# Performance work log

Measured on AMD Instinct MI355X. Metric: run time of the kernel, lower is better.

Reference implementation:

```python
import jax, jax.numpy as jnp
import numpy as np

B, C, H, W = 4, 512, 64, 64
CQ = C // 4  # query/key channels


def setup_inputs() -> dict:
    key = jax.random.key(0)
    ks = jax.random.split(key, 8)
    s_in = 1.0 / np.sqrt(C)
    return {
        "x": jax.random.normal(ks[0], (B, C, H, W), dtype=jnp.float32),
        "Wf_w": jax.random.normal(ks[1], (CQ, C), dtype=jnp.float32) * s_in,
        "Wf_b": jax.random.normal(ks[2], (CQ,), dtype=jnp.float32) * 0.01,
        "Wh_w": jax.random.normal(ks[3], (CQ, C), dtype=jnp.float32) * s_in,
        "Wh_b": jax.random.normal(ks[4], (CQ,), dtype=jnp.float32) * 0.01,
        "Wl_w": jax.random.normal(ks[5], (C, C), dtype=jnp.float32) * s_in,
        "Wl_b": jax.random.normal(ks[6], (C,), dtype=jnp.float32) * 0.01,
        "alpha": jax.random.uniform(ks[7], (1,), dtype=jnp.float32),
    }


def reference(x, Wf_w, Wf_b, Wh_w, Wh_b, Wl_w, Wl_b, alpha):
    b, c, h, w = x.shape
    n = h * w
    xr = x.reshape(b, c, n)  # (B, C, N)
    # 1x1 convs == per-pixel linear projections
    f = jnp.einsum('oc,bcn->bon', Wf_w, xr) + Wf_b[None, :, None]  # (B, C/4, N)
    k = jnp.einsum('oc,bcn->bon', Wh_w, xr) + Wh_b[None, :, None]  # (B, C/4, N)
    v = jnp.einsum('oc,bcn->bon', Wl_w, xr) + Wl_b[None, :, None]  # (B, C,   N)
    # t[b, i, j] = <f[:, i], k[:, j]>  -> (B, N, N)
    scores = jnp.einsum('boi,boj->bij', f, k)
    att = jax.nn.softmax(scores, axis=-1)
    # out[b, c, i] = sum_j v[b, c, j] * att[b, i, j]  (bmm with att^T)
    out = jnp.einsum('bcj,bij->bci', v, att)
    out = out.reshape(b, c, h, w)
    return out * alpha[0] + x
```

## Files before the change

kernel.cpp:

```cpp
#include <hip/hip_runtime.h>
#include <hip/hip_bf16.h>

typedef _Float16 f16;
typedef _Float16 f16x4 __attribute__((ext_vector_type(4)));
typedef _Float16 f16x8 __attribute__((ext_vector_type(8)));
typedef float f32x4 __attribute__((ext_vector_type(4)));
typedef float f32x16 __attribute__((ext_vector_type(16)));

constexpr int BATCH = 4, C = 512, CQ = 128, N = 4096;
constexpr int FKD = 256;

constexpr size_t WS_XT   = 0;
constexpr size_t WS_FT   = WS_XT   + (size_t)BATCH * N * C * 2;
constexpr size_t WS_KT   = WS_FT   + (size_t)BATCH * N * CQ * 2;
constexpr size_t WS_V    = WS_KT   + (size_t)BATCH * N * CQ * 2;
constexpr size_t WS_WCAT = WS_V    + (size_t)BATCH * C * N * 2;
constexpr size_t WS_WL   = WS_WCAT + (size_t)FKD * C * 2;
constexpr size_t WS_BC   = WS_WL   + (size_t)C * C * 2;

__global__ void prep_weights(const float* __restrict__ Wf_w, const float* __restrict__ Wf_b,
                             const float* __restrict__ Wh_w, const float* __restrict__ Wh_b,
                             const float* __restrict__ Wl_w,
                             f16* __restrict__ wcat, f16* __restrict__ wl, float* __restrict__ bcat) {
    int i = blockIdx.x * 256 + threadIdx.x;
    if (i < FKD * C) {
        int o = i >> 9, c = i & 511;
        float v = (o < CQ) ? Wf_w[o * C + c] : Wh_w[(o - CQ) * C + c];
        wcat[i] = (f16)v;
    }
    if (i < C * C) wl[i] = (f16)Wl_w[i];
    if (i < FKD) bcat[i] = (i < CQ) ? Wf_b[i] : Wh_b[i - CQ];
}

__global__ void transpose_x(const float* __restrict__ x, f16* __restrict__ xt) {
    __shared__ float tile[64][65];
    int gid = blockIdx.x;
    int b = gid >> 9, rem = gid & 511;
    int c0 = (rem >> 6) * 64, n0 = (rem & 63) * 64;
    int t = threadIdx.x;
    int tn = t & 63, tg = t >> 6;
    const float* xp = x + (size_t)b * C * N + (size_t)c0 * N + n0;
#pragma unroll
    for (int r = 0; r < 16; ++r) {
        int cl = tg + r * 4;
        tile[cl][tn] = xp[(size_t)cl * N + tn];
    }
    __syncthreads();
    f16* xo = xt + (size_t)b * N * C + (size_t)n0 * C + c0;
#pragma unroll
    for (int r = 0; r < 16; ++r) {
        int nl = tg + r * 4;
        xo[(size_t)nl * C + tn] = (f16)tile[tn][nl];
    }
}

__global__ void __launch_bounds__(256) proj_fk(const f16* __restrict__ xt, const f16* __restrict__ wcat,
                                               const float* __restrict__ bcat,
                                               f16* __restrict__ ft, f16* __restrict__ kt) {
    int wid = blockIdx.x * 4 + (threadIdx.x >> 6);
    int lane = threadIdx.x & 63;
    int li = lane & 15, lg = lane >> 4;
    int b  = wid >> 8;
    int nt = (wid >> 2) & 63;
    int ot = wid & 3;
    int n0 = nt * 64, o0 = ot * 64;
    const f16* ap = xt + (size_t)(b * N + n0 + li) * C + lg * 8;
    const f16* bp = wcat + (size_t)(o0 + li) * C + lg * 8;
    f32x4 acc[4][4] = {};
    for (int ks = 0; ks < 16; ++ks) {
        f16x8 a4[4], b4[4];
#pragma unroll
        for (int t = 0; t < 4; ++t) a4[t] = *(const f16x8*)(ap + (size_t)(t * 16) * C + ks * 32);
#pragma unroll
        for (int t = 0; t < 4; ++t) b4[t] = *(const f16x8*)(bp + (size_t)(t * 16) * C + ks * 32);
#pragma unroll
        for (int tA = 0; tA < 4; ++tA)
#pragma unroll
            for (int tB = 0; tB < 4; ++tB)
                acc[tA][tB] = __builtin_amdgcn_mfma_f32_16x16x32_f16(a4[tA], b4[tB], acc[tA][tB], 0, 0, 0);
    }
#pragma unroll
    for (int tB = 0; tB < 4; ++tB) {
        int o = o0 + tB * 16 + li;
        float bias = bcat[o];
        if (o < CQ) {
#pragma unroll
            for (int tA = 0; tA < 4; ++tA)
#pragma unroll
                for (int r = 0; r < 4; ++r) {
                    int n = n0 + tA * 16 + lg * 4 + r;
                    ft[((size_t)(b * N + n)) * CQ + o] = (f16)(acc[tA][tB][r] + bias);
                }
        } else {
            int ck = o - CQ;
#pragma unroll
            for (int tA = 0; tA < 4; ++tA)
#pragma unroll
                for (int r = 0; r < 4; ++r) {
                    int n = n0 + tA * 16 + lg * 4 + r;
                    kt[(((size_t)b * (N >> 2) + (n >> 2)) * 4 + (n & 3)) * 128 + ck] = (f16)(acc[tA][tB][r] + bias);
                }
        }
    }
}

__global__ void __launch_bounds__(256) proj_v(const f16* __restrict__ xt, const f16* __restrict__ wl,
                                              const float* __restrict__ wlb, f16* __restrict__ v) {
    int wid = blockIdx.x * 4 + (threadIdx.x >> 6);
    int lane = threadIdx.x & 63;
    int li = lane & 15, lg = lane >> 4;
    int b  = wid >> 9;
    int ct = (wid >> 6) & 7;
    int nt = wid & 63;
    int c0 = ct * 64, n0 = nt * 64;
    const f16* ap = wl + (size_t)(c0 + li) * C + lg * 8;
    const f16* bp = xt + (size_t)(b * N + n0 + li) * C + lg * 8;
    f32x4 acc[4][4] = {};
    for (int ks = 0; ks < 16; ++ks) {
        f16x8 a4[4], b4[4];
#pragma unroll
        for (int t = 0; t < 4; ++t) a4[t] = *(const f16x8*)(ap + (size_t)(t * 16) * C + ks * 32);
#pragma unroll
        for (int t = 0; t < 4; ++t) b4[t] = *(const f16x8*)(bp + (size_t)(t * 16) * C + ks * 32);
#pragma unroll
        for (int tA = 0; tA < 4; ++tA)
#pragma unroll
            for (int tB = 0; tB < 4; ++tB)
                acc[tA][tB] = __builtin_amdgcn_mfma_f32_16x16x32_f16(a4[tA], b4[tB], acc[tA][tB], 0, 0, 0);
    }
#pragma unroll
    for (int tA = 0; tA < 4; ++tA)
#pragma unroll
        for (int r = 0; r < 4; ++r) {
            int c = c0 + tA * 16 + lg * 4 + r;
            float bias = wlb[c];
            const size_t cpb = ((size_t)b * 32 + (c >> 4)) * 512;
            const int cl = c & 15;
#pragma unroll
            for (int tB = 0; tB < 4; ++tB) {
                int n = n0 + tB * 16 + li;
                v[(cpb + (n >> 3)) * 128 + cl * 8 + (n & 7)] = (f16)(acc[tA][tB][r] + bias);
            }
        }
}

__global__ void __launch_bounds__(512, 2) attn(const f16* __restrict__ ft, const f16* __restrict__ kt,
                                               const f16* __restrict__ v,
                                               const float* __restrict__ x, const float* __restrict__ alphap,
                                               float* __restrict__ out) {
    __shared__ __align__(16) f16 kbuf[2][128 * 128];
    __shared__ __align__(16) f16 pbuf[64 * 128];
    __shared__ float smax[4][2][32];
    __shared__ float ssum[4][2][32];

    const int tid  = threadIdx.x;
    const int wv   = tid >> 6;
    const int lane = tid & 63;
    const int li = lane & 15, lg = lane >> 4;
    const int l31 = lane & 31, lh = lane >> 5;
    const int sw = l31 & 7;
    const int wj = wv & 3;
    const int wi = wv >> 2;
    const int v0 = blockIdx.x;
    const int b  = (v0 & 7) >> 1;
    const int it = ((v0 & 1) << 5) | (v0 >> 3);
    const int i0 = it * 64;

    f16x8 fb[8];
    {
        const f16* fp = ft + (size_t)(b * N + i0 + wi * 32 + l31) * CQ + lh * 8;
#pragma unroll
        for (int ks = 0; ks < 8; ++ks) fb[ks] = *(const f16x8*)(fp + ks * 16);
    }

    const f16* ktb = kt + (size_t)b * N * 128;
    {
#pragma unroll
        for (int k = 0; k < 4; ++k) {
            f16x8 vv = *(const f16x8*)(ktb + (((size_t)(wv * 4 + k)) * 4 + lg) * 128 + li * 8);
            *(f16x8*)(&kbuf[0][(wv * 16 + k * 4 + lg) * 128 + ((li ^ ((k * 4 + lg) & 7)) * 8)]) = vv;
        }
    }

    const f16* vL = v + (((size_t)b * 32 + wj * 8 + (l31 >> 4)) * 512 + lh) * 128 + (l31 & 15) * 8;
    const int prow = wi * 32 + l31;
    f32x16 oacc[4] = {};
    float ms = -1e30f, ls = 0.f;
    __syncthreads();

    for (int t = 0; t < 32; ++t) {
        const f16* kc = &kbuf[t & 1][0];
        f16*       kn = &kbuf[(t + 1) & 1][0];
        const int gn = (t < 31) ? (t + 1) * 32 : 0;
        f16x8 stg[4];
#pragma unroll
        for (int k = 0; k < 4; ++k)
            stg[k] = *(const f16x8*)(ktb + (((size_t)(gn + wv * 4 + k)) * 4 + lg) * 128 + li * 8);

        f32x16 s = {};
        __builtin_amdgcn_s_setprio(1);
#pragma unroll
        for (int ks = 0; ks < 8; ++ks) {
            f16x8 kf = *(const f16x8*)(&kc[(wj * 32 + l31) * 128 + (((ks * 2 + lh) ^ sw) * 8)]);
            s = __builtin_amdgcn_mfma_f32_32x32x16_f16(kf, fb[ks], s, 0, 0, 0);
        }
        __builtin_amdgcn_s_setprio(0);

        float tm = s[0];
#pragma unroll
        for (int r = 1; r < 16; ++r) tm = fmaxf(tm, s[r]);
        tm = fmaxf(tm, __shfl_xor(tm, 32));
        if (lane < 32) smax[wj][wi][l31] = tm;
        f16x8 vaA[4], vaB[4];
#pragma unroll
        for (int ct = 0; ct < 4; ++ct) vaA[ct] = *(const f16x8*)(vL + ((size_t)(ct * 1024 + t * 16)) * 128);
        __syncthreads();
        float gm = fmaxf(fmaxf(smax[0][wi][l31], smax[1][wi][l31]),
                         fmaxf(smax[2][wi][l31], smax[3][wi][l31]));
        if (!__all(gm <= ms + 8.0f)) {
            float mn = fmaxf(ms, gm), sc = __expf(ms - mn);
            ms = mn; ls *= sc;
#pragma unroll
            for (int ct = 0; ct < 4; ++ct) oacc[ct] *= sc;
        }
#pragma unroll
        for (int ct = 0; ct < 4; ++ct) vaB[ct] = *(const f16x8*)(vL + ((size_t)(ct * 1024 + t * 16 + 2)) * 128);
        float psum = 0.f;
#pragma unroll
        for (int q = 0; q < 4; ++q) {
            f16x4 pk;
#pragma unroll
            for (int r = 0; r < 4; ++r) { float p = __expf(s[q * 4 + r] - ms); psum += p; pk[r] = (f16)p; }
            const int g = (wj * 4 + q) ^ sw;
            *(f16x4*)(&pbuf[prow * 128 + g * 8 + lh * 4]) = pk;
        }
        psum += __shfl_xor(psum, 32);
        if (lane < 32) ssum[wj][wi][l31] = psum;
#pragma unroll
        for (int k = 0; k < 4; ++k)
            *(f16x8*)(&kn[(wv * 16 + k * 4 + lg) * 128 + ((li ^ ((k * 4 + lg) & 7)) * 8)]) = stg[k];
        __syncthreads();
        ls += ssum[0][wi][l31] + ssum[1][wi][l31] + ssum[2][wi][l31] + ssum[3][wi][l31];
#pragma unroll
        for (int js = 0; js < 8; ++js) {
            f16x8 pb = *(const f16x8*)(&pbuf[prow * 128 + (((js * 2 + lh) ^ sw) * 8)]);
            f16x8 vv0, vv1, vv2, vv3;
            if (js & 1) { vv0 = vaB[0]; vv1 = vaB[1]; vv2 = vaB[2]; vv3 = vaB[3]; }
            else        { vv0 = vaA[0]; vv1 = vaA[1]; vv2 = vaA[2]; vv3 = vaA[3]; }
            if (js < 6) {
#pragma unroll
                for (int ct = 0; ct < 4; ++ct) {
                    f16x8 nv = *(const f16x8*)(vL + ((size_t)(ct * 1024 + t * 16 + (js + 2) * 2)) * 128);
                    if (js & 1) vaB[ct] = nv; else vaA[ct] = nv;
                }
            }
            __builtin_amdgcn_s_setprio(1);
            oacc[0] = __builtin_amdgcn_mfma_f32_32x32x16_f16(vv0, pb, oacc[0], 0, 0, 0);
            oacc[1] = __builtin_amdgcn_mfma_f32_32x32x16_f16(vv1, pb, oacc[1], 0, 0, 0);
            oacc[2] = __builtin_amdgcn_mfma_f32_32x32x16_f16(vv2, pb, oacc[2], 0, 0, 0);
            oacc[3] = __builtin_amdgcn_mfma_f32_32x32x16_f16(vv3, pb, oacc[3], 0, 0, 0);
            __builtin_amdgcn_s_setprio(0);
        }
    }

    const float alpha = alphap[0];
    const float inv = alpha / ls;
    const int icol = i0 + wi * 32 + l31;
#pragma unroll
    for (int ct = 0; ct < 4; ++ct)
#pragma unroll
        for (int r = 0; r < 16; ++r) {
            const int c = wj * 128 + ct * 32 + (r & 3) + 8 * (r >> 2) + 4 * lh;
            const size_t off = (size_t)(b * C + c) * N + icol;
            out[off] = oacc[ct][r] * inv + x[off];
        }
}

extern "C" void kernel_launch(void* const* d_in, const int* in_sizes, int n_in,
                              void* d_out, int out_size, void* d_ws, size_t ws_size,
                              hipStream_t stream) {
    const float* x     = (const float*)d_in[0];
    const float* Wf_w  = (const float*)d_in[1];
    const float* Wf_b  = (const float*)d_in[2];
    const float* Wh_w  = (const float*)d_in[3];
    const float* Wh_b  = (const float*)d_in[4];
    const float* Wl_w  = (const float*)d_in[5];
    const float* Wl_b  = (const float*)d_in[6];
    const float* alpha = (const float*)d_in[7];
    char* ws = (char*)d_ws;
    f16*   xt   = (f16*)(ws + WS_XT);
    f16*   ftb  = (f16*)(ws + WS_FT);
    f16*   ktb  = (f16*)(ws + WS_KT);
    f16*   vb   = (f16*)(ws + WS_V);
    f16*   wcat = (f16*)(ws + WS_WCAT);
    f16*   wl   = (f16*)(ws + WS_WL);
    float* bcat = (float*)(ws + WS_BC);
    float* out  = (float*)d_out;

    prep_weights<<<dim3((C * C + 255) / 256), dim3(256), 0, stream>>>(Wf_w, Wf_b, Wh_w, Wh_b, Wl_w, wcat, wl, bcat);
    transpose_x<<<dim3(BATCH * 8 * 64), dim3(256), 0, stream>>>(x, xt);
    proj_fk<<<dim3(256), dim3(256), 0, stream>>>(xt, wcat, bcat, ftb, ktb);
    proj_v<<<dim3(512), dim3(256), 0, stream>>>(xt, wl, Wl_b, vb);
    attn<<<dim3(256), dim3(512), 0, stream>>>(ftb, ktb, vb, x, alpha, out);
}
```

Before: 190.3 us.

## Restructure attention into 1024-thread blocks with 256-key tiles and direct-to-LDS K loads

The attention kernel moves to 16 waves per block and processes 256 keys per iteration, so the key loop runs 16 times instead of 32. K tiles are loaded straight into a single LDS buffer with global_load_lds instead of going through registers into a double buffer. Each wave now owns 32 output channels across both 64-query halves, so each V fragment is loaded once and used for two MFMAs instead of being loaded twice by separate waves. In exchange, LDS use and per-wave softmax bookkeeping go up, and the single K buffer depends on the barrier placement to keep the next-tile load from racing with current reads.

```diff
diff --git a/kernel.cpp b/kernel.cpp
--- a/kernel.cpp
+++ b/kernel.cpp
@@ -17,6 +17,9 @@
 constexpr size_t WS_WCAT = WS_V    + (size_t)BATCH * C * N * 2;
 constexpr size_t WS_WL   = WS_WCAT + (size_t)FKD * C * 2;
 constexpr size_t WS_BC   = WS_WL   + (size_t)C * C * 2;
+
+#define AS1(p) ((const __attribute__((address_space(1))) void*)(p))
+#define AS3(p) ((__attribute__((address_space(3))) void*)(p))
 
 __global__ void prep_weights(const float* __restrict__ Wf_w, const float* __restrict__ Wf_b,
                              const float* __restrict__ Wh_w, const float* __restrict__ Wh_b,
@@ -144,14 +147,14 @@
         }
 }
 
-__global__ void __launch_bounds__(512, 2) attn(const f16* __restrict__ ft, const f16* __restrict__ kt,
-                                               const f16* __restrict__ v,
-                                               const float* __restrict__ x, const float* __restrict__ alphap,
-                                               float* __restrict__ out) {
-    __shared__ __align__(16) f16 kbuf[2][128 * 128];
-    __shared__ __align__(16) f16 pbuf[64 * 128];
-    __shared__ float smax[4][2][32];
-    __shared__ float ssum[4][2][32];
+__global__ void __launch_bounds__(1024, 1) attn(const f16* __restrict__ ft, const f16* __restrict__ kt,
+                                                const f16* __restrict__ v,
+                                                const float* __restrict__ x, const float* __restrict__ alphap,
+                                                float* __restrict__ out) {
+    __shared__ __align__(16) f16 kbuf[256 * 128];
+    __shared__ __align__(16) f16 pbuf[64 * 256];
+    __shared__ float smax[8][2][32];
+    __shared__ float ssum[8][2][32];
 
     const int tid  = threadIdx.x;
     const int wv   = tid >> 6;
@@ -159,8 +162,8 @@
     const int li = lane & 15, lg = lane >> 4;
     const int l31 = lane & 31, lh = lane >> 5;
     const int sw = l31 & 7;
-    const int wj = wv & 3;
-    const int wi = wv >> 2;
+    const int wj = wv & 7;
+    const int wi = wv >> 3;
     const int v0 = blockIdx.x;
     const int b  = (v0 & 7) >> 1;
     const int it = ((v0 & 1) << 5) | (v0 >> 3);
@@ -174,106 +177,99 @@
     }
 
     const f16* ktb = kt + (size_t)b * N * 128;
-    {
+    auto STAGE = [&](int tile) {
 #pragma unroll
         for (int k = 0; k < 4; ++k) {
-            f16x8 vv = *(const f16x8*)(ktb + (((size_t)(wv * 4 + k)) * 4 + lg) * 128 + li * 8);
-            *(f16x8*)(&kbuf[0][(wv * 16 + k * 4 + lg) * 128 + ((li ^ ((k * 4 + lg) & 7)) * 8)]) = vv;
-        }
-    }
-
-    const f16* vL = v + (((size_t)b * 32 + wj * 8 + (l31 >> 4)) * 512 + lh) * 128 + (l31 & 15) * 8;
+            const f16* gsrc = ktb + (((size_t)(tile * 64 + wv * 4 + k)) * 4 + lg) * 128
+                                  + ((li ^ ((k * 4 + lg) & 7)) * 8);
+            __builtin_amdgcn_global_load_lds(AS1(gsrc), AS3(&kbuf[(wv * 16 + k * 4) * 128]), 16, 0, 0);
+        }
+    };
+
+    STAGE(0);
+    const f16* vL = v + (((size_t)b * 32 + wv * 2 + (l31 >> 4)) * 512 + lh) * 128 + (l31 & 15) * 8;
     const int prow = wi * 32 + l31;
-    f32x16 oacc[4] = {};
-    float ms = -1e30f, ls = 0.f;
+    f32x16 oacc[2] = {};
+    float ms[2] = {-1e30f, -1e30f}, ls[2] = {0.f, 0.f};
     __syncthreads();
 
-    for (int t = 0; t < 32; ++t) {
-        const f16* kc = &kbuf[t & 1][0];
-        f16*       kn = &kbuf[(t + 1) & 1][0];
-        const int gn = (t < 31) ? (t + 1) * 32 : 0;
-        f16x8 stg[4];
-#pragma unroll
-        for (int k = 0; k < 4; ++k)
-            stg[k] = *(const f16x8*)(ktb + (((size_t)(gn + wv * 4 + k)) * 4 + lg) * 128 + li * 8);
-
+    for (int t = 0; t < 16; ++t) {
         f32x16 s = {};
         __builtin_amdgcn_s_setprio(1);
 #pragma unroll
         for (int ks = 0; ks < 8; ++ks) {
-            f16x8 kf = *(const f16x8*)(&kc[(wj * 32 + l31) * 128 + (((ks * 2 + lh) ^ sw) * 8)]);
+            f16x8 kf = *(const f16x8*)(&kbuf[(wj * 32 + l31) * 128 + (((ks * 2 + lh) ^ sw) * 8)]);
             s = __builtin_amdgcn_mfma_f32_32x32x16_f16(kf, fb[ks], s, 0, 0, 0);
         }
         __builtin_amdgcn_s_setprio(0);
-
         float tm = s[0];
 #pragma unroll
         for (int r = 1; r < 16; ++r) tm = fmaxf(tm, s[r]);
         tm = fmaxf(tm, __shfl_xor(tm, 32));
         if (lane < 32) smax[wj][wi][l31] = tm;
-        f16x8 vaA[4], vaB[4];
-#pragma unroll
-        for (int ct = 0; ct < 4; ++ct) vaA[ct] = *(const f16x8*)(vL + ((size_t)(ct * 1024 + t * 16)) * 128);
         __syncthreads();
-        float gm = fmaxf(fmaxf(smax[0][wi][l31], smax[1][wi][l31]),
-                         fmaxf(smax[2][wi][l31], smax[3][wi][l31]));
-        if (!__all(gm <= ms + 8.0f)) {
-            float mn = fmaxf(ms, gm), sc = __expf(ms - mn);
-            ms = mn; ls *= sc;
-#pragma unroll
-            for (int ct = 0; ct < 4; ++ct) oacc[ct] *= sc;
-        }
-#pragma unroll
-        for (int ct = 0; ct < 4; ++ct) vaB[ct] = *(const f16x8*)(vL + ((size_t)(ct * 1024 + t * 16 + 2)) * 128);
+        if (t < 15) STAGE(t + 1);
+#pragma unroll
+        for (int h = 0; h < 2; ++h) {
+            float gm = smax[0][h][l31];
+#pragma unroll
+            for (int w = 1; w < 8; ++w) gm = fmaxf(gm, smax[w][h][l31]);
+            if (!__all(gm <= ms[h] + 8.0f)) {
+                float mn = fmaxf(ms[h], gm), sc = __expf(ms[h] - mn);
+                ms[h] = mn; ls[h] *= sc;
+                oacc[h] *= sc;
+            }
+        }
         float psum = 0.f;
 #pragma unroll
         for (int q = 0; q < 4; ++q) {
             f16x4 pk;
 #pragma unroll
-            for (int r = 0; r < 4; ++r) { float p = __expf(s[q * 4 + r] - ms); psum += p; pk[r] = (f16)p; }
+            for (int r = 0; r < 4; ++r) { float p = __expf(s[q * 4 + r] - ms[wi]); psum += p; pk[r] = (f16)p; }
             const int g = (wj * 4 + q) ^ sw;
-            *(f16x4*)(&pbuf[prow * 128 + g * 8 + lh * 4]) = pk;
+            *(f16x4*)(&pbuf[prow * 256 + g * 8 + lh * 4]) = pk;
         }
         psum += __shfl_xor(psum, 32);
         if (lane < 32) ssum[wj][wi][l31] = psum;
-#pragma unroll
-        for (int k = 0; k < 4; ++k)
-            *(f16x8*)(&kn[(wv * 16 + k * 4 + lg) * 128 + ((li ^ ((k * 4 + lg) & 7)) * 8)]) = stg[k];
+        f16x8 vaA, vaB;
+        vaA = *(const f16x8*)(vL + ((size_t)(t * 32)) * 128);
+        vaB = *(const f16x8*)(vL + ((size_t)(t * 32 + 2)) * 128);
         __syncthreads();
-        ls += ssum[0][wi][l31] + ssum[1][wi][l31] + ssum[2][wi][l31] + ssum[3][wi][l31];
-#pragma unroll
-        for (int js = 0; js < 8; ++js) {
-            f16x8 pb = *(const f16x8*)(&pbuf[prow * 128 + (((js * 2 + lh) ^ sw) * 8)]);
-            f16x8 vv0, vv1, vv2, vv3;
-            if (js & 1) { vv0 = vaB[0]; vv1 = vaB[1]; vv2 = vaB[2]; vv3 = vaB[3]; }
-            else        { vv0 = vaA[0]; vv1 = vaA[1]; vv2 = vaA[2]; vv3 = vaA[3]; }
-            if (js < 6) {
-#pragma unroll
-                for (int ct = 0; ct < 4; ++ct) {
-                    f16x8 nv = *(const f16x8*)(vL + ((size_t)(ct * 1024 + t * 16 + (js + 2) * 2)) * 128);
-                    if (js & 1) vaB[ct] = nv; else vaA[ct] = nv;
-                }
+#pragma unroll
+        for (int h = 0; h < 2; ++h) {
+            float a0 = 0.f;
+#pragma unroll
+            for (int w = 0; w < 8; ++w) a0 += ssum[w][h][l31];
+            ls[h] += a0;
+        }
+#pragma unroll
+        for (int js = 0; js < 16; ++js) {
+            f16x8 vv = (js & 1) ? vaB : vaA;
+            if (js < 14) {
+                f16x8 nv = *(const f16x8*)(vL + ((size_t)(t * 32 + (js + 2) * 2)) * 128);
+                if (js & 1) vaB = nv; else vaA = nv;
             }
+            f16x8 pb0 = *(const f16x8*)(&pbuf[l31 * 256 + (((js * 2 + lh) ^ sw) * 8)]);
+            f16x8 pb1 = *(const f16x8*)(&pbuf[(32 + l31) * 256 + (((js * 2 + lh) ^ sw) * 8)]);
             __builtin_amdgcn_s_setprio(1);
-            oacc[0] = __builtin_amdgcn_mfma_f32_32x32x16_f16(vv0, pb, oacc[0], 0, 0, 0);
-            oacc[1] = __builtin_amdgcn_mfma_f32_32x32x16_f16(vv1, pb, oacc[1], 0, 0, 0);
-            oacc[2] = __builtin_amdgcn_mfma_f32_32x32x16_f16(vv2, pb, oacc[2], 0, 0, 0);
-            oacc[3] = __builtin_amdgcn_mfma_f32_32x32x16_f16(vv3, pb, oacc[3], 0, 0, 0);
+            oacc[0] = __builtin_amdgcn_mfma_f32_32x32x16_f16(vv, pb0, oacc[0], 0, 0, 0);
+            oacc[1] = __builtin_amdgcn_mfma_f32_32x32x16_f16(vv, pb1, oacc[1], 0, 0, 0);
             __builtin_amdgcn_s_setprio(0);
         }
     }
 
     const float alpha = alphap[0];
-    const float inv = alpha / ls;
-    const int icol = i0 + wi * 32 + l31;
-#pragma unroll
-    for (int ct = 0; ct < 4; ++ct)
+#pragma unroll
+    for (int h = 0; h < 2; ++h) {
+        const float inv = alpha / ls[h];
+        const int icol = i0 + h * 32 + l31;
 #pragma unroll
         for (int r = 0; r < 16; ++r) {
-            const int c = wj * 128 + ct * 32 + (r & 3) + 8 * (r >> 2) + 4 * lh;
+            const int c = wv * 32 + (r & 3) + 8 * (r >> 2) + 4 * lh;
             const size_t off = (size_t)(b * C + c) * N + icol;
-            out[off] = oacc[ct][r] * inv + x[off];
-        }
+            out[off] = oacc[h][r] * inv + x[off];
+        }
+    }
 }
 
 extern "C" void kernel_launch(void* const* d_in, const int* in_sizes, int n_in,
@@ -301,5 +297,5 @@
     transpose_x<<<dim3(BATCH * 8 * 64), dim3(256), 0, stream>>>(x, xt);
     proj_fk<<<dim3(256), dim3(256), 0, stream>>>(xt, wcat, bcat, ftb, ktb);
     proj_v<<<dim3(512), dim3(256), 0, stream>>>(xt, wl, Wl_b, vb);
-    attn<<<dim3(256), dim3(512), 0, stream>>>(ftb, ktb, vb, x, alpha, out);
-}
+    attn<<<dim3(256), dim3(1024), 0, stream>>>(ftb, ktb, vb, x, alpha, out);
+}
```

Result: slower. 214.4 us (+12.7%).
